# Performance work log

Measured on AMD Instinct MI355X. Metric: run time of the kernel, lower is better.

The kernel has to match this reference:

```python
import jax, jax.numpy as jnp
import numpy as np
from jax import lax

KS = 3           # kernel size
PAD = 1          # padding
BN_EPS = 1e-5


def _conv(x, w, b):
    # plain stride-1, pad-1 NCHW conv
    y = lax.conv_general_dilated(x, w, window_strides=(1, 1),
                                 padding=[(PAD, PAD), (PAD, PAD)],
                                 dimension_numbers=("NCHW", "OIHW", "NCHW"))
    return y + b[None, :, None, None]


def _deform_conv(x, offset, mask, w_reg):
    # x: [B,C,H,W]; offset: [B,2K,H,W] (dy,dx interleaved); mask: [B,K,H,W]
    B, C, H, W = x.shape
    K = KS * KS
    dy = offset[:, 0::2]  # [B,K,H,W]
    dx = offset[:, 1::2]
    base_ky = jnp.repeat(jnp.arange(KS), KS).astype(x.dtype)   # [K]
    base_kx = jnp.tile(jnp.arange(KS), KS).astype(x.dtype)
    gy = (jnp.arange(H) - PAD).astype(x.dtype)
    gx = (jnp.arange(W) - PAD).astype(x.dtype)
    py = base_ky[None, :, None, None] + gy[None, None, :, None] + dy  # [B,K,H,W]
    px = base_kx[None, :, None, None] + gx[None, None, None, :] + dx

    y0 = jnp.floor(py); x0 = jnp.floor(px)
    wy = py - y0;       wx = px - x0
    x_flat = x.reshape(B, C, H * W)

    def gather(yi, xi):
        valid = (yi >= 0) & (yi < H) & (xi >= 0) & (xi < W)
        yc = jnp.clip(yi, 0, H - 1).astype(jnp.int32)
        xc = jnp.clip(xi, 0, W - 1).astype(jnp.int32)
        idx = (yc * W + xc).reshape(B, 1, K * H * W)
        v = jnp.take_along_axis(x_flat, jnp.broadcast_to(idx, (B, C, K * H * W)), axis=2)
        v = v.reshape(B, C, K, H, W)
        return v * valid[:, None].astype(x.dtype)

    sampled = ((1 - wy) * (1 - wx))[:, None] * gather(y0, x0) \
            + ((1 - wy) * wx)[:, None]       * gather(y0, x0 + 1) \
            + (wy * (1 - wx))[:, None]       * gather(y0 + 1, x0) \
            + (wy * wx)[:, None]             * gather(y0 + 1, x0 + 1)
    sampled = sampled * mask[:, None]  # modulation, [B,C,K,H,W]
    Cout = w_reg.shape[0]
    return jnp.einsum("bckhw,ock->bohw", sampled, w_reg.reshape(Cout, C, K))


def setup_inputs() -> dict:
    key = jax.random.key(0)
    ks = jax.random.split(key, 9)
    B, Cin, Cout, H, W = 4, 256, 256, 64, 64
    K = KS * KS
    inp = {
        "x": jax.random.normal(ks[0], (B, Cin, H, W), jnp.float32),
        # offset / modulator conv params (zero-init in source; small random for meaningful test)
        "w_off": jax.random.normal(ks[1], (2 * K, Cin, KS, KS), jnp.float32) * 0.01,
        "b_off": jax.random.normal(ks[2], (2 * K,), jnp.float32) * 0.01,
        "w_mod": jax.random.normal(ks[3], (K, Cin, KS, KS), jnp.float32) * 0.01,
        "b_mod": jax.random.normal(ks[4], (K,), jnp.float32) * 0.01,
        # regular conv weight (bias=False)
        "w_reg": jax.random.normal(ks[5], (Cout, Cin, KS, KS), jnp.float32) * (1.0 / np.sqrt(Cin * K)),
        # BatchNorm (inference mode: running stats)
        "gamma": jnp.ones((Cout,), jnp.float32),
        "beta": jnp.zeros((Cout,), jnp.float32),
        "run_mean": jax.random.normal(ks[6], (Cout,), jnp.float32) * 0.1,
        "run_var": jax.random.uniform(ks[7], (Cout,), jnp.float32, 0.5, 1.5),
    }
    return inp


def reference(x, w_off, b_off, w_mod, b_mod, w_reg, gamma, beta, run_mean, run_var):
    offset = _conv(x, w_off, b_off)                       # [B,2K,H,W]
    mask = 2.0 * jax.nn.sigmoid(_conv(x, w_mod, b_mod))   # [B,K,H,W]
    y = _deform_conv(x, offset, mask, w_reg)              # [B,Cout,H,W]
    inv = gamma / jnp.sqrt(run_var + BN_EPS)
    y = y * inv[None, :, None, None] + (beta - run_mean * inv)[None, :, None, None]
    return jax.nn.relu(y)
```

## Files before the change

### kernel.cpp

```cpp
#include <hip/hip_runtime.h>
#include <hip/hip_bf16.h>

typedef unsigned short u16;
typedef unsigned int   u32;
typedef short   bf16x8 __attribute__((ext_vector_type(8)));
typedef float   f32x4  __attribute__((ext_vector_type(4)));

__device__ __forceinline__ float bf2f(u16 u) {
    u32 t = ((u32)u) << 16;
    return __builtin_bit_cast(float, t);
}
__device__ __forceinline__ u32 f2bf(float f) {
    u32 u = __builtin_bit_cast(u32, f);
    return (u + 0x7FFFu + ((u >> 16) & 1u)) >> 16;
}
__device__ __forceinline__ void load_lds16(const u16* g, u16* l) {
    __builtin_amdgcn_global_load_lds(
        (const __attribute__((address_space(1))) u32*)(const void*)g,
        (__attribute__((address_space(3))) u32*)(void*)l, 16, 0, 0);
}
__device__ __forceinline__ uint4 gload4(const u16* sbase, u32 voff) {
    uint4 r;
    asm volatile("global_load_dwordx4 %0, %1, %2"
                 : "=v"(r) : "v"(voff), "s"(sbase) : "memory");
    return r;
}
__device__ __forceinline__ f32x4 gload4f(const float* sbase, u32 voff) {
    f32x4 r;
    asm volatile("global_load_dwordx4 %0, %1, %2"
                 : "=v"(r) : "v"(voff), "s"(sbase) : "memory");
    return r;
}
#define WAITVM(N) do { asm volatile("s_waitcnt vmcnt(" #N ")" ::: "memory"); \
                       __builtin_amdgcn_sched_barrier(0); } while (0)


__global__ void kprep(const float* __restrict__ woff, const float* __restrict__ wmod,
                      u16* __restrict__ ah, u16* __restrict__ al) {
    int i = blockIdx.x * 256 + threadIdx.x;
    if (i >= 32 * 2304) return;
    int oc = i / 2304, r = i - oc * 2304;
    int t = r >> 8, c = r & 255;
    float v = 0.f;
    if (oc < 18)      v = woff[oc * 2304 + c * 9 + t];
    else if (oc < 27) v = wmod[(oc - 18) * 2304 + c * 9 + t];
    u32 hb = f2bf(v);
    u32 lb = f2bf(v - bf2f((u16)hb));
    ah[i] = (u16)hb;
    al[i] = (u16)lb;
}

__global__ void kwreg(const float* __restrict__ wreg, u16* __restrict__ wregb) {
    int i = blockIdx.x * 256 + threadIdx.x;
    int o = i / 2304, r = i - o * 2304;
    int t = r >> 8, c = r & 255;
    wregb[i] = (u16)f2bf(wreg[o * 2304 + c * 9 + t]);
}

__global__ __launch_bounds__(256) void ktrans(const float* __restrict__ x,
                                              float* __restrict__ xt) {
    __shared__ float T[64][65];
    int t = threadIdx.x;
    int pl = t & 63, cr = t >> 6;
    int p0 = blockIdx.x * 64;
    int c0 = blockIdx.y * 64;
    int b  = blockIdx.z;
    const float* xb  = x  + ((long)b << 20);
    float*       xtb = xt + ((long)b << 20);
#pragma unroll
    for (int i = 0; i < 16; i++) {
        int c = cr + i * 4;
        T[c][pl] = xb[((long)(c0 + c) << 12) + p0 + pl];
    }
    __syncthreads();
#pragma unroll
    for (int i = 0; i < 16; i++) {
        int p = cr + i * 4;
        xtb[(long)(p0 + p) * 256 + c0 + pl] = T[pl][p];
    }
}

__global__ __launch_bounds__(256) void koffg(const float* __restrict__ xt,
                                             const u16* __restrict__ ah_g,
                                             const u16* __restrict__ al_g,
                                             const float* __restrict__ boff,
                                             const float* __restrict__ bmod,
                                             float* __restrict__ offf) {
    __shared__ u16 Ah[2][32 * 72], Al[2][32 * 72];
    __shared__ u16 Bh[2][32 * 72], Bl[2][32 * 72];
    int tid = threadIdx.x;
    int bid = blockIdx.x;
    int xcd = bid & 7, j = bid >> 3;
    int img = xcd >> 1;
    int row = ((xcd & 1) << 5) + (j >> 1);
    int n0 = ((img << 6) + row) * 64 + (j & 1) * 32;
    int b = n0 >> 12, h0 = (n0 & 4095) >> 6, w0 = n0 & 63;
    int lane = tid & 63, wv = tid >> 6;
    int mt = wv & 1, nt = wv >> 1;
    int col = lane & 15, quad = lane >> 4;

    int aoc = tid >> 3, ak0 = (tid & 7) * 8;
    int chq = lane & 15, pxs = lane >> 4;
    int px0 = wv * 4 + pxs, px1 = px0 + 16;

    const float* xtb = xt + ((long)b << 20);
    u32 avoff0 = (u32)(aoc * 2304 + ak0) * 2;

    f32x4 acc = (f32x4){0.f, 0.f, 0.f, 0.f};

    uint4 pah, pal;
    f32x4 xa, xc;
    bool  vma, vmb;

    auto issue = [&](int kt) {
        int t = kt >> 2, c0 = (kt & 3) << 6, r0 = kt * 64;
        int dy = t / 3 - 1, dx = t % 3 - 1;
        pah = gload4(ah_g, avoff0 + (u32)r0 * 2);
        pal = gload4(al_g, avoff0 + (u32)r0 * 2);
        int hp = h0 + dy;
        bool vh = (unsigned)hp < 64u;
        int hc = min(max(hp, 0), 63);
        u32 cb = (u32)(c0 + chq * 4) << 2;
        int wpa = w0 + px0 + dx;
        vma = vh && ((unsigned)wpa < 64u);
        int wca = min(max(wpa, 0), 63);
        xa = gload4f(xtb, ((u32)(hc * 64 + wca) << 10) + cb);
        int wpb = w0 + px1 + dx;
        vmb = vh && ((unsigned)wpb < 64u);
        int wcb = min(max(wpb, 0), 63);
        xc = gload4f(xtb, ((u32)(hc * 64 + wcb) << 10) + cb);
    };
    auto stores = [&](int buf) {
        *(uint4*)&Ah[buf][aoc * 72 + ak0] = pah;
        *(uint4*)&Al[buf][aoc * 72 + ak0] = pal;
        u32 wh[2], wl[2];
#pragma unroll
        for (int i = 0; i < 4; i++) {
            float v = vma ? xa[i] : 0.f;
            u32 hb = f2bf(v);
            u32 lb = f2bf(v - bf2f((u16)hb));
            if (i & 1) { wh[i >> 1] |= hb << 16; wl[i >> 1] |= lb << 16; }
            else       { wh[i >> 1]  = hb;       wl[i >> 1]  = lb; }
        }
        *(uint2*)&Bh[buf][px0 * 72 + chq * 4] = make_uint2(wh[0], wh[1]);
        *(uint2*)&Bl[buf][px0 * 72 + chq * 4] = make_uint2(wl[0], wl[1]);
#pragma unroll
        for (int i = 0; i < 4; i++) {
            float v = vmb ? xc[i] : 0.f;
            u32 hb = f2bf(v);
            u32 lb = f2bf(v - bf2f((u16)hb));
            if (i & 1) { wh[i >> 1] |= hb << 16; wl[i >> 1] |= lb << 16; }
            else       { wh[i >> 1]  = hb;       wl[i >> 1]  = lb; }
        }
        *(uint2*)&Bh[buf][px1 * 72 + chq * 4] = make_uint2(wh[0], wh[1]);
        *(uint2*)&Bl[buf][px1 * 72 + chq * 4] = make_uint2(wl[0], wl[1]);
    };

    issue(0);
    WAITVM(0);
    stores(0);
    issue(1);
    asm volatile("s_waitcnt lgkmcnt(0)" ::: "memory");
    __builtin_amdgcn_s_barrier();
    __builtin_amdgcn_sched_barrier(0);

    for (int kt = 0; kt < 36; kt++) {
        int cur = kt & 1, nxt = kt + 1;
#pragma unroll
        for (int ks = 0; ks < 2; ks++) {
            int ko = ks * 32 + quad * 8;
            bf16x8 fah = *(const bf16x8*)&Ah[cur][(mt * 16 + col) * 72 + ko];
            bf16x8 fal = *(const bf16x8*)&Al[cur][(mt * 16 + col) * 72 + ko];
            bf16x8 fbh = *(const bf16x8*)&Bh[cur][(nt * 16 + col) * 72 + ko];
            bf16x8 fbl = *(const bf16x8*)&Bl[cur][(nt * 16 + col) * 72 + ko];
            acc = __builtin_amdgcn_mfma_f32_16x16x32_bf16(fah, fbh, acc, 0, 0, 0);
            acc = __builtin_amdgcn_mfma_f32_16x16x32_bf16(fah, fbl, acc, 0, 0, 0);
            acc = __builtin_amdgcn_mfma_f32_16x16x32_bf16(fal, fbh, acc, 0, 0, 0);
        }
        if (nxt < 36) {
            WAITVM(0);
            stores(nxt & 1);
            if (nxt + 1 < 36) issue(nxt + 1);
        }
        asm volatile("s_waitcnt lgkmcnt(0)" ::: "memory");
        __builtin_amdgcn_s_barrier();
        __builtin_amdgcn_sched_barrier(0);
    }

    int n = n0 + nt * 16 + col;
#pragma unroll
    for (int r = 0; r < 4; r++) {
        int oc = mt * 16 + quad * 4 + r;
        float s = acc[r];
        if (oc < 18) {
            int ch = 3 * (oc >> 1) + (oc & 1);
            offf[(ch << 14) + n] = s + boff[oc];
        } else if (oc < 27) {
            float tt = s + bmod[oc - 18];
            int ch = 3 * (oc - 18) + 2;
            offf[(ch << 14) + n] = 2.f / (1.f + __expf(-tt));
        }
    }
}

__global__ __launch_bounds__(512, 4) void kfused(const float* __restrict__ xt,
                                                 const float* __restrict__ offf,
                                                 const u16* __restrict__ wregb,
                                                 const float* __restrict__ gamma,
                                                 const float* __restrict__ beta,
                                                 const float* __restrict__ rmean,
                                                 const float* __restrict__ rvar,
                                                 float* __restrict__ out) {
    __shared__ u16 Wl[2][256 * 64];
    __shared__ u16 Sl[2][8 * 32 * 8];
    int tid = threadIdx.x;
    int lane = tid & 63, wv = tid >> 6;
    int chq = lane & 15;
    int plo = wv * 4 + (lane >> 4);
    int bid = blockIdx.x;
    int xcd = bid & 7, jj = bid >> 3;
    int bb  = xcd >> 1;
    int h   = ((xcd & 1) << 5) + (jj >> 1);
    int nbase = ((bb << 6) + h) * 64 + (jj & 1) * 32;
    int wo = wv * 32;
    int col = lane & 15, quad = lane >> 4;

    const float* xb = xt + ((long)bb << 20);

    f32x4 acc[2][2];
#pragma unroll
    for (int i = 0; i < 2; i++)
#pragma unroll
        for (int j = 0; j < 2; j++) acc[i][j] = (f32x4){0.f, 0.f, 0.f, 0.f};

    u32   pb[4];
    float sw[4];
    f32x4 g[4];

    auto tapcomp = [&](int t) {
        int n = nbase + plo;
        int w = n & 63;
        int gy = t / 3, tx = t - 3 * gy;
        float dy = offf[((3 * t + 0) << 14) + n];
        float dx = offf[((3 * t + 1) << 14) + n];
        float m  = offf[((3 * t + 2) << 14) + n];
        float py = (float)(h - 1 + gy) + dy;
        float px = (float)(w - 1 + tx) + dx;
        float y0f = floorf(py), x0f = floorf(px);
        float wy = py - y0f, wx = px - x0f;
        int iy0 = (int)y0f, ix0 = (int)x0f;
        int iy1 = iy0 + 1, ix1 = ix0 + 1;
        bool vy0 = (unsigned)iy0 < 64u, vy1 = (unsigned)iy1 < 64u;
        bool vx0 = (unsigned)ix0 < 64u, vx1 = (unsigned)ix1 < 64u;
        int cy0 = min(max(iy0, 0), 63), cy1 = min(max(iy1, 0), 63);
        int cx0 = min(max(ix0, 0), 63), cx1 = min(max(ix1, 0), 63);
        pb[0] = (u32)(cy0 * 64 + cx0) << 10; pb[1] = (u32)(cy0 * 64 + cx1) << 10;
        pb[2] = (u32)(cy1 * 64 + cx0) << 10; pb[3] = (u32)(cy1 * 64 + cx1) << 10;
        float a = 1.f - wy, bw = 1.f - wx;
        sw[0] = (vy0 && vx0) ? a  * bw * m : 0.f;
        sw[1] = (vy0 && vx1) ? a  * wx * m : 0.f;
        sw[2] = (vy1 && vx0) ? wy * bw * m : 0.f;
        sw[3] = (vy1 && vx1) ? wy * wx * m : 0.f;
    };
    auto gissue = [&](int kt) {
        u32 co = ((u32)(kt & 3) << 8) + (u32)chq * 16;
#pragma unroll
        for (int nb = 0; nb < 4; nb++) g[nb] = gload4f(xb, pb[nb] + co);
    };
    auto dmaA = [&](int kt, int buf) {
#pragma unroll
        for (int i = 0; i < 4; i++) {
            int cidx = tid + i * 512;
            int o = cidx >> 3, qp = cidx & 7;
            int ql = qp ^ (o & 7);
            load_lds16(wregb + (long)o * 2304 + kt * 64 + ql * 8,
                       &Wl[buf][cidx * 8]);
        }
    };
    auto bwrite = [&](int buf) {
        f32x4 v = sw[0] * g[0] + sw[1] * g[1] + sw[2] * g[2] + sw[3] * g[3];
        u32 w0 = f2bf(v[0]) | (f2bf(v[1]) << 16);
        u32 w1 = f2bf(v[2]) | (f2bf(v[3]) << 16);
        *(uint2*)&Sl[buf][((chq >> 1) * 32 + plo) * 8 + (chq & 1) * 4] =
            make_uint2(w0, w1);
    };

    tapcomp(0);
    gissue(0);
    dmaA(0, 0);
    WAITVM(0);
    bwrite(0);
    __syncthreads();

    for (int kt = 0; kt < 36; kt++) {
        int cur = kt & 1, nxt = kt + 1;
        if (nxt < 36) {
            if ((nxt & 3) == 0) tapcomp(nxt >> 2);
            gissue(nxt);
            dmaA(nxt, nxt & 1);
        }
#pragma unroll
        for (int ks = 0; ks < 2; ks++) {
            bf16x8 af[2], bfr[2];
#pragma unroll
            for (int i = 0; i < 2; i++) {
                int r = wo + i * 16 + col;
                int ph = (ks * 4 + quad) ^ (r & 7);
                af[i] = *(const bf16x8*)&Wl[cur][r * 64 + ph * 8];
            }
#pragma unroll
            for (int j = 0; j < 2; j++)
                bfr[j] = *(const bf16x8*)&Sl[cur][((ks * 4 + quad) * 32 +
                                                   (j * 16 + col)) * 8];
#pragma unroll
            for (int i = 0; i < 2; i++)
#pragma unroll
                for (int j = 0; j < 2; j++)
                    acc[i][j] = __builtin_amdgcn_mfma_f32_16x16x32_bf16(
                        af[i], bfr[j], acc[i][j], 0, 0, 0);
        }
        if (nxt < 36) {
            WAITVM(4);
            bwrite(nxt & 1);
        }
        __syncthreads();
    }

#pragma unroll
    for (int i = 0; i < 2; i++) {
        int ob = wo + i * 16 + quad * 4;
        float inv[4], add[4];
#pragma unroll
        for (int r = 0; r < 4; r++) {
            int o = ob + r;
            float iv = gamma[o] * rsqrtf(rvar[o] + 1e-5f);
            inv[r] = iv; add[r] = beta[o] - rmean[o] * iv;
        }
#pragma unroll
        for (int j = 0; j < 2; j++) {
            int n_g = nbase + j * 16 + col;
            int bq = n_g >> 12, hw = n_g & 4095;
            float* op = out + ((long)bq << 20) + hw;
#pragma unroll
            for (int r = 0; r < 4; r++) {
                float v = acc[i][j][r] * inv[r] + add[r];
                v = fmaxf(v, 0.f);
                op[(long)(ob + r) << 12] = v;
            }
        }
    }
}

extern "C" void kernel_launch(void* const* d_in, const int* in_sizes, int n_in,
                              void* d_out, int out_size, void* d_ws, size_t ws_size,
                              hipStream_t stream) {
    const float* x     = (const float*)d_in[0];
    const float* woff  = (const float*)d_in[1];
    const float* boff  = (const float*)d_in[2];
    const float* wmod  = (const float*)d_in[3];
    const float* bmod  = (const float*)d_in[4];
    const float* wreg  = (const float*)d_in[5];
    const float* gamma = (const float*)d_in[6];
    const float* beta  = (const float*)d_in[7];
    const float* rmean = (const float*)d_in[8];
    const float* rvar  = (const float*)d_in[9];
    float* out = (float*)d_out;

    char* ws = (char*)d_ws;
    u16*   wph   = (u16*)(ws);
    u16*   wpl   = (u16*)(ws + 0x40000u);
    float* offf  = (float*)(ws + 0x80000u);
    u16*   wregb = (u16*)(ws + 0x240000u);
    float* xt    = (float*)(ws + 0x400000u);

    kprep<<<288,  256, 0, stream>>>(woff, wmod, wph, wpl);
    kwreg<<<2304, 256, 0, stream>>>(wreg, wregb);
    ktrans<<<dim3(64, 4, 4), 256, 0, stream>>>(x, xt);
    koffg<<<512,  256, 0, stream>>>(xt, wph, wpl, boff, bmod, offf);
    kfused<<<512, 512, 0, stream>>>(xt, offf, wregb, gamma, beta,
                                    rmean, rvar, out);
}
```

Before: 175.1 us.

## Split koffg K-loop across two 256-thread groups with LDS reduction

```diff
diff --git a/kernel.cpp b/kernel.cpp
--- a/kernel.cpp
+++ b/kernel.cpp
@@ -80,15 +80,16 @@
     }
 }
 
-__global__ __launch_bounds__(256) void koffg(const float* __restrict__ xt,
-                                             const u16* __restrict__ ah_g,
-                                             const u16* __restrict__ al_g,
-                                             const float* __restrict__ boff,
-                                             const float* __restrict__ bmod,
-                                             float* __restrict__ offf) {
-    __shared__ u16 Ah[2][32 * 72], Al[2][32 * 72];
-    __shared__ u16 Bh[2][32 * 72], Bl[2][32 * 72];
+__global__ __launch_bounds__(512, 4) void koffg(const float* __restrict__ xt,
+                                                const u16* __restrict__ ah_g,
+                                                const u16* __restrict__ al_g,
+                                                const float* __restrict__ boff,
+                                                const float* __restrict__ bmod,
+                                                float* __restrict__ offf) {
+    __shared__ u16 Ah[4][32 * 72], Al[4][32 * 72];
+    __shared__ u16 Bh[4][32 * 72], Bl[4][32 * 72];
     int tid = threadIdx.x;
+    int ltid = tid & 255, kg = tid >> 8;
     int bid = blockIdx.x;
     int xcd = bid & 7, j = bid >> 3;
     int img = xcd >> 1;
@@ -96,12 +97,14 @@
     int n0 = ((img << 6) + row) * 64 + (j & 1) * 32;
     int b = n0 >> 12, h0 = (n0 & 4095) >> 6, w0 = n0 & 63;
     int lane = tid & 63, wv = tid >> 6;
-    int mt = wv & 1, nt = wv >> 1;
+    int mt = wv & 1, nt = (wv >> 1) & 1;
     int col = lane & 15, quad = lane >> 4;
 
-    int aoc = tid >> 3, ak0 = (tid & 7) * 8;
+    int aoc = ltid >> 3, ak0 = (ltid & 7) * 8;
     int chq = lane & 15, pxs = lane >> 4;
-    int px0 = wv * 4 + pxs, px1 = px0 + 16;
+    int px0 = (wv & 3) * 4 + pxs, px1 = px0 + 16;
+
+    int ktb = kg * 18;
 
     const float* xtb = xt + ((long)b << 20);
     u32 avoff0 = (u32)(aoc * 2304 + ak0) * 2;
@@ -131,8 +134,9 @@
         xc = gload4f(xtb, ((u32)(hc * 64 + wcb) << 10) + cb);
     };
     auto stores = [&](int buf) {
-        *(uint4*)&Ah[buf][aoc * 72 + ak0] = pah;
-        *(uint4*)&Al[buf][aoc * 72 + ak0] = pal;
+        int sb = kg * 2 + buf;
+        *(uint4*)&Ah[sb][aoc * 72 + ak0] = pah;
+        *(uint4*)&Al[sb][aoc * 72 + ak0] = pal;
         u32 wh[2], wl[2];
 #pragma unroll
         for (int i = 0; i < 4; i++) {
@@ -142,8 +146,8 @@
             if (i & 1) { wh[i >> 1] |= hb << 16; wl[i >> 1] |= lb << 16; }
             else       { wh[i >> 1]  = hb;       wl[i >> 1]  = lb; }
         }
-        *(uint2*)&Bh[buf][px0 * 72 + chq * 4] = make_uint2(wh[0], wh[1]);
-        *(uint2*)&Bl[buf][px0 * 72 + chq * 4] = make_uint2(wl[0], wl[1]);
+        *(uint2*)&Bh[sb][px0 * 72 + chq * 4] = make_uint2(wh[0], wh[1]);
+        *(uint2*)&Bl[sb][px0 * 72 + chq * 4] = make_uint2(wl[0], wl[1]);
 #pragma unroll
         for (int i = 0; i < 4; i++) {
             float v = vmb ? xc[i] : 0.f;
@@ -152,53 +156,61 @@
             if (i & 1) { wh[i >> 1] |= hb << 16; wl[i >> 1] |= lb << 16; }
             else       { wh[i >> 1]  = hb;       wl[i >> 1]  = lb; }
         }
-        *(uint2*)&Bh[buf][px1 * 72 + chq * 4] = make_uint2(wh[0], wh[1]);
-        *(uint2*)&Bl[buf][px1 * 72 + chq * 4] = make_uint2(wl[0], wl[1]);
-    };
-
-    issue(0);
+        *(uint2*)&Bh[sb][px1 * 72 + chq * 4] = make_uint2(wh[0], wh[1]);
+        *(uint2*)&Bl[sb][px1 * 72 + chq * 4] = make_uint2(wl[0], wl[1]);
+    };
+
+    issue(ktb + 0);
     WAITVM(0);
     stores(0);
-    issue(1);
+    issue(ktb + 1);
     asm volatile("s_waitcnt lgkmcnt(0)" ::: "memory");
     __builtin_amdgcn_s_barrier();
     __builtin_amdgcn_sched_barrier(0);
 
-    for (int kt = 0; kt < 36; kt++) {
+    for (int kt = 0; kt < 18; kt++) {
         int cur = kt & 1, nxt = kt + 1;
+        int sb = kg * 2 + cur;
 #pragma unroll
         for (int ks = 0; ks < 2; ks++) {
             int ko = ks * 32 + quad * 8;
-            bf16x8 fah = *(const bf16x8*)&Ah[cur][(mt * 16 + col) * 72 + ko];
-            bf16x8 fal = *(const bf16x8*)&Al[cur][(mt * 16 + col) * 72 + ko];
-            bf16x8 fbh = *(const bf16x8*)&Bh[cur][(nt * 16 + col) * 72 + ko];
-            bf16x8 fbl = *(const bf16x8*)&Bl[cur][(nt * 16 + col) * 72 + ko];
+            bf16x8 fah = *(const bf16x8*)&Ah[sb][(mt * 16 + col) * 72 + ko];
+            bf16x8 fal = *(const bf16x8*)&Al[sb][(mt * 16 + col) * 72 + ko];
+            bf16x8 fbh = *(const bf16x8*)&Bh[sb][(nt * 16 + col) * 72 + ko];
+            bf16x8 fbl = *(const bf16x8*)&Bl[sb][(nt * 16 + col) * 72 + ko];
             acc = __builtin_amdgcn_mfma_f32_16x16x32_bf16(fah, fbh, acc, 0, 0, 0);
             acc = __builtin_amdgcn_mfma_f32_16x16x32_bf16(fah, fbl, acc, 0, 0, 0);
             acc = __builtin_amdgcn_mfma_f32_16x16x32_bf16(fal, fbh, acc, 0, 0, 0);
         }
-        if (nxt < 36) {
+        if (nxt < 18) {
             WAITVM(0);
             stores(nxt & 1);
-            if (nxt + 1 < 36) issue(nxt + 1);
+            if (nxt + 1 < 18) issue(ktb + nxt + 1);
         }
         asm volatile("s_waitcnt lgkmcnt(0)" ::: "memory");
         __builtin_amdgcn_s_barrier();
         __builtin_amdgcn_sched_barrier(0);
     }
 
-    int n = n0 + nt * 16 + col;
-#pragma unroll
-    for (int r = 0; r < 4; r++) {
-        int oc = mt * 16 + quad * 4 + r;
-        float s = acc[r];
-        if (oc < 18) {
-            int ch = 3 * (oc >> 1) + (oc & 1);
-            offf[(ch << 14) + n] = s + boff[oc];
-        } else if (oc < 27) {
-            float tt = s + bmod[oc - 18];
-            int ch = 3 * (oc - 18) + 2;
-            offf[(ch << 14) + n] = 2.f / (1.f + __expf(-tt));
+    float* scratch = (float*)&Ah[0][0];
+    if (kg) *(f32x4*)&scratch[ltid * 4] = acc;
+    __syncthreads();
+    if (kg == 0) {
+        f32x4 o = *(const f32x4*)&scratch[ltid * 4];
+        acc += o;
+        int n = n0 + nt * 16 + col;
+#pragma unroll
+        for (int r = 0; r < 4; r++) {
+            int oc = mt * 16 + quad * 4 + r;
+            float s = acc[r];
+            if (oc < 18) {
+                int ch = 3 * (oc >> 1) + (oc & 1);
+                offf[(ch << 14) + n] = s + boff[oc];
+            } else if (oc < 27) {
+                float tt = s + bmod[oc - 18];
+                int ch = 3 * (oc - 18) + 2;
+                offf[(ch << 14) + n] = 2.f / (1.f + __expf(-tt));
+            }
         }
     }
 }
@@ -376,7 +388,7 @@
     kprep<<<288,  256, 0, stream>>>(woff, wmod, wph, wpl);
     kwreg<<<2304, 256, 0, stream>>>(wreg, wregb);
     ktrans<<<dim3(64, 4, 4), 256, 0, stream>>>(x, xt);
-    koffg<<<512,  256, 0, stream>>>(xt, wph, wpl, boff, bmod, offf);
+    koffg<<<512,  512, 0, stream>>>(xt, wph, wpl, boff, bmod, offf);
     kfused<<<512, 512, 0, stream>>>(xt, offf, wregb, gamma, beta,
                                     rmean, rvar, out);
 }
```

Measured after the change: 176.9 us. No clear change (+1.0%).
